# Optimization experiments

Measured on AMD Instinct MI355X. Metric: run time of the kernel, lower is better.

The kernel has to match this reference:

```python
import jax, jax.numpy as jnp
import numpy as np

EPS = 1e-7


def ciou_pairwise(b1, b2):
    # b1: (N,1,4), b2: (1,N,4) in xyxy; returns (N,N) CIoU
    b1x1, b1y1, b1x2, b1y2 = b1[..., 0], b1[..., 1], b1[..., 2], b1[..., 3]
    b2x1, b2y1, b2x2, b2y2 = b2[..., 0], b2[..., 1], b2[..., 2], b2[..., 3]

    # intersection
    iw = jnp.clip(jnp.minimum(b1x2, b2x2) - jnp.maximum(b1x1, b2x1), 0.0)
    ih = jnp.clip(jnp.minimum(b1y2, b2y2) - jnp.maximum(b1y1, b2y1), 0.0)
    inter = iw * ih

    w1, h1 = b1x2 - b1x1, b1y2 - b1y1
    w2, h2 = b2x2 - b2x1, b2y2 - b2y1
    union = w1 * h1 + w2 * h2 - inter + EPS
    iou = inter / union

    # smallest enclosing box diagonal
    cw = jnp.maximum(b1x2, b2x2) - jnp.minimum(b1x1, b2x1)
    ch = jnp.maximum(b1y2, b2y2) - jnp.minimum(b1y1, b2y1)
    c2 = cw * cw + ch * ch + EPS

    # squared center distance
    rho2 = ((b2x1 + b2x2 - b1x1 - b1x2) ** 2 + (b2y1 + b2y2 - b1y1 - b1y2) ** 2) / 4.0

    # aspect-ratio consistency term
    v = (4.0 / (np.pi ** 2)) * (jnp.arctan(w2 / (h2 + EPS)) - jnp.arctan(w1 / (h1 + EPS))) ** 2
    alpha = jax.lax.stop_gradient(v / (v - iou + (1.0 + EPS)))
    return iou - (rho2 / c2 + v * alpha)


def setup_inputs() -> dict:
    key = jax.random.key(0)
    k1, k2, k3 = jax.random.split(key, 3)
    N = 4096
    conf = jax.random.uniform(k1, (N, 1), dtype=jnp.float32)           # confidence in [0,1)
    xy1 = jax.random.uniform(k2, (N, 2), dtype=jnp.float32) * 600.0    # top-left corner
    wh = jax.random.uniform(k3, (N, 2), dtype=jnp.float32) * 100.0 + 1.0  # width/height >= 1
    x = jnp.concatenate([conf, xy1, xy1 + wh], axis=1)                 # (N, 5): conf, x1, y1, x2, y2
    gamma = jnp.zeros((1,), dtype=jnp.float32)
    return {"x": x, "gamma": gamma}


def reference(x, gamma):
    boxes = x[:, 1:]
    conf = x[:, 0]
    iou = ciou_pairwise(boxes[:, None, :], boxes[None, :, :])          # (N, N)
    conf_matrix = conf[:, None] * conf[None, :]                        # (N, N) outer product
    attention = jax.nn.softmax(iou * conf_matrix, axis=-1)             # (N, N)
    x_prime = x * gamma + attention @ x                                # (N, 5)
    return jax.nn.sigmoid(x_prime)
```

## Files before the change

kernel.cpp:

```cpp
#include <hip/hip_runtime.h>
#include <math.h>

#define N 4096
#define FEPS 1e-7f
#define HEPS 5e-8f
#define BLK 256
#define JT 64
#define CH 64
#define NPAIR (CH / 2)
#define KATAN 0.6366197723675814f
#define SQL2E 1.2011224087864498f

typedef float v2f __attribute__((ext_vector_type(2)));


__device__ __forceinline__ v2f min2(v2f a, v2f b) {
    v2f r; r.x = fminf(a.x, b.x); r.y = fminf(a.y, b.y); return r;
}
__device__ __forceinline__ v2f max2(v2f a, v2f b) {
    v2f r; r.x = fmaxf(a.x, b.x); r.y = fmaxf(a.y, b.y); return r;
}
__device__ __forceinline__ v2f rcp2(v2f a) {
    v2f r; r.x = __builtin_amdgcn_rcpf(a.x); r.y = __builtin_amdgcn_rcpf(a.y); return r;
}
__device__ __forceinline__ v2f exp22(v2f a) {
    v2f r; r.x = __builtin_amdgcn_exp2f(a.x); r.y = __builtin_amdgcn_exp2f(a.y); return r;
}

__global__ __launch_bounds__(BLK) void ciou_attn_kernel(
        const float* __restrict__ x,
        float* __restrict__ part) {
    __shared__ float jrec[NPAIR * 24];
    const int tid = threadIdx.x;
    const int gb = blockIdx.x / JT;
    const int jt = blockIdx.x % JT;
    const int i = gb * BLK + tid;

    if (tid < CH) {
        int j = jt * CH + tid;
        float cf = x[j * 5 + 0], jx1 = x[j * 5 + 1], jy1 = x[j * 5 + 2];
        float jx2 = x[j * 5 + 3], jy2 = x[j * 5 + 4];
        float w = jx2 - jx1, h = jy2 - jy1;
        float* dp = &jrec[(tid >> 1) * 24 + (tid & 1)];
        dp[0]  = jx1;               dp[2]  = jy1;
        dp[4]  = jx2;               dp[6]  = jy2;
        dp[8]  = (jx1 + jx2) * 0.5f; dp[10] = (jy1 + jy2) * 0.5f;
        dp[12] = w;                 dp[14] = h;
        dp[16] = fmaf(w, h, HEPS);
        dp[18] = KATAN * atanf(w / (h + FEPS));
        dp[20] = cf * SQL2E;        dp[22] = cf;
    }

    const float rx1 = x[i * 5 + 1], ry1 = x[i * 5 + 2];
    const float rx2 = x[i * 5 + 3], ry2 = x[i * 5 + 4];
    const float rw = rx2 - rx1, rh = ry2 - ry1;
    const float rhx = (rx1 + rx2) * 0.5f, rhy = (ry1 + ry2) * 0.5f;
    const float rareps = fmaf(rw, rh, HEPS);
    const float rat = KATAN * atanf(rw / (rh + FEPS));
    const float rcf2 = x[i * 5 + 0] * SQL2E;

    __syncthreads();

    v2f sum = 0.f, a0 = 0.f, a1 = 0.f, a2 = 0.f, a3 = 0.f, a4 = 0.f;
    const float ONEP = 1.f + FEPS;

#pragma unroll 4
    for (int p = 0; p < NPAIR; p++) {
        const float* f = &jrec[p * 24];
        const v2f X1 = *(const v2f*)(f + 0),  Y1 = *(const v2f*)(f + 2);
        const v2f X2 = *(const v2f*)(f + 4),  Y2 = *(const v2f*)(f + 6);
        const v2f HX = *(const v2f*)(f + 8),  HY = *(const v2f*)(f + 10);
        const v2f W  = *(const v2f*)(f + 12), H  = *(const v2f*)(f + 14);
        const v2f AR = *(const v2f*)(f + 16), AT = *(const v2f*)(f + 18);
        const v2f CF2 = *(const v2f*)(f + 20), CF = *(const v2f*)(f + 22);

        v2f iwr = min2(rx2, X2) - max2(rx1, X1);
        v2f ihr = min2(ry2, Y2) - max2(ry1, Y1);
        v2f inter = max2(iwr, 0.f) * max2(ihr, 0.f);
        v2f uni = (rareps + AR) - inter;
        v2f cw = (rw + W) - iwr;
        v2f chh = (rh + H) - ihr;
        v2f c2 = cw * cw + chh * chh + FEPS;
        v2f dx = HX - rhx;
        v2f dy = HY - rhy;
        v2f rho2 = dx * dx + dy * dy;
        v2f da = AT - rat;
        v2f v = da * da;
        v2f P = (v + ONEP) * uni - inter;
        P = max2(P, 1e-12f);
        v2f rr = rcp2(uni * c2 * P);
        v2f t1 = inter * c2 - rho2 * uni;
        v2f vu = v * uni;
        v2f num = t1 * P - (vu * vu) * c2;
        v2f e = exp22((num * rr) * (rcf2 * CF2));
        sum += e;
        a0 += e * CF;
        a1 += e * X1;
        a2 += e * Y1;
        a3 += e * X2;
        a4 += e * Y2;
    }

    float* p = part + (size_t)jt * 6 * N;
    p[0 * N + i] = sum.x + sum.y;
    p[1 * N + i] = a0.x + a0.y;
    p[2 * N + i] = a1.x + a1.y;
    p[3 * N + i] = a2.x + a2.y;
    p[4 * N + i] = a3.x + a3.y;
    p[5 * N + i] = a4.x + a4.y;
}

__global__ void epilogue_kernel(const float* __restrict__ x,
                                const float* __restrict__ gamma,
                                const float* __restrict__ part,
                                float* __restrict__ out) {
    int idx = blockIdx.x * blockDim.x + threadIdx.x;
    if (idx >= N * 5) return;
    int c = idx / N, i = idx - c * N;
    float se = 0.f, a = 0.f;
#pragma unroll 8
    for (int jt = 0; jt < JT; jt++) {
        const float* p = part + (size_t)jt * 6 * N;
        se += p[0 * N + i];
        a  += p[(1 + c) * N + i];
    }
    float xp = x[i * 5 + c] * gamma[0] + a / se;
    out[i * 5 + c] = 1.f / (1.f + expf(-xp));
}

extern "C" void kernel_launch(void* const* d_in, const int* in_sizes, int n_in,
                              void* d_out, int out_size, void* d_ws, size_t ws_size,
                              hipStream_t stream) {
    const float* x = (const float*)d_in[0];
    const float* gamma = (const float*)d_in[1];
    float* out = (float*)d_out;
    float* part = (float*)d_ws;

    ciou_attn_kernel<<<(N / BLK) * JT, BLK, 0, stream>>>(x, part);
    epilogue_kernel<<<(N * 5 + 255) / 256, 256, 0, stream>>>(x, gamma, part, out);
}
```

Measured before the change: 81.27 us.

## Shrink shared j-record and split epilogue reduction across four waves

The per-j shared-memory record is reduced from 12 to 6 pairs. Width, height, centre and area are now recomputed in the inner loop from the corner coordinates, and the raw confidence is recovered by rescaling the pre-scaled one after the loop. This trades a few extra ALU ops per pair for fewer LDS reads. The epilogue now splits the 64 partial tiles across four waves per output group and combines them with a shared-memory reduction, which adds parallelism and memory-level concurrency to the partial sums.

Measured after the change: 77.47 us (median of 2 runs). 4.7% less time.

```diff
diff --git a/kernel.cpp b/kernel.cpp
--- a/kernel.cpp
+++ b/kernel.cpp
@@ -10,6 +10,7 @@
 #define NPAIR (CH / 2)
 #define KATAN 0.6366197723675814f
 #define SQL2E 1.2011224087864498f
+#define ISQL2E 0.8325546111576977f
 
 typedef float v2f __attribute__((ext_vector_type(2)));
 
@@ -30,7 +31,7 @@
 __global__ __launch_bounds__(BLK) void ciou_attn_kernel(
         const float* __restrict__ x,
         float* __restrict__ part) {
-    __shared__ float jrec[NPAIR * 24];
+    __shared__ float jrec[NPAIR * 12];
     const int tid = threadIdx.x;
     const int gb = blockIdx.x / JT;
     const int jt = blockIdx.x % JT;
@@ -40,15 +41,10 @@
         int j = jt * CH + tid;
         float cf = x[j * 5 + 0], jx1 = x[j * 5 + 1], jy1 = x[j * 5 + 2];
         float jx2 = x[j * 5 + 3], jy2 = x[j * 5 + 4];
-        float w = jx2 - jx1, h = jy2 - jy1;
-        float* dp = &jrec[(tid >> 1) * 24 + (tid & 1)];
-        dp[0]  = jx1;               dp[2]  = jy1;
-        dp[4]  = jx2;               dp[6]  = jy2;
-        dp[8]  = (jx1 + jx2) * 0.5f; dp[10] = (jy1 + jy2) * 0.5f;
-        dp[12] = w;                 dp[14] = h;
-        dp[16] = fmaf(w, h, HEPS);
-        dp[18] = KATAN * atanf(w / (h + FEPS));
-        dp[20] = cf * SQL2E;        dp[22] = cf;
+        float* dp = &jrec[(tid >> 1) * 12 + (tid & 1)];
+        dp[0]  = jx1;  dp[2] = jy1;  dp[4] = jx2;  dp[6] = jy2;
+        dp[8]  = KATAN * atanf((jx2 - jx1) / ((jy2 - jy1) + FEPS));
+        dp[10] = cf * SQL2E;
     }
 
     const float rx1 = x[i * 5 + 1], ry1 = x[i * 5 + 2];
@@ -66,13 +62,13 @@
 
 #pragma unroll 4
     for (int p = 0; p < NPAIR; p++) {
-        const float* f = &jrec[p * 24];
+        const float* f = &jrec[p * 12];
         const v2f X1 = *(const v2f*)(f + 0),  Y1 = *(const v2f*)(f + 2);
         const v2f X2 = *(const v2f*)(f + 4),  Y2 = *(const v2f*)(f + 6);
-        const v2f HX = *(const v2f*)(f + 8),  HY = *(const v2f*)(f + 10);
-        const v2f W  = *(const v2f*)(f + 12), H  = *(const v2f*)(f + 14);
-        const v2f AR = *(const v2f*)(f + 16), AT = *(const v2f*)(f + 18);
-        const v2f CF2 = *(const v2f*)(f + 20), CF = *(const v2f*)(f + 22);
+        const v2f AT = *(const v2f*)(f + 8),  CF2 = *(const v2f*)(f + 10);
+        const v2f W = X2 - X1, H = Y2 - Y1;
+        const v2f HX = (X1 + X2) * 0.5f, HY = (Y1 + Y2) * 0.5f;
+        const v2f AR = W * H + HEPS;
 
         v2f iwr = min2(rx2, X2) - max2(rx1, X1);
         v2f ihr = min2(ry2, Y2) - max2(ry1, Y1);
@@ -94,7 +90,7 @@
         v2f num = t1 * P - (vu * vu) * c2;
         v2f e = exp22((num * rr) * (rcf2 * CF2));
         sum += e;
-        a0 += e * CF;
+        a0 += e * CF2;
         a1 += e * X1;
         a2 += e * Y1;
         a3 += e * X2;
@@ -103,7 +99,7 @@
 
     float* p = part + (size_t)jt * 6 * N;
     p[0 * N + i] = sum.x + sum.y;
-    p[1 * N + i] = a0.x + a0.y;
+    p[1 * N + i] = (a0.x + a0.y) * ISQL2E;
     p[2 * N + i] = a1.x + a1.y;
     p[3 * N + i] = a2.x + a2.y;
     p[4 * N + i] = a3.x + a3.y;
@@ -114,18 +110,27 @@
                                 const float* __restrict__ gamma,
                                 const float* __restrict__ part,
                                 float* __restrict__ out) {
-    int idx = blockIdx.x * blockDim.x + threadIdx.x;
-    if (idx >= N * 5) return;
-    int c = idx / N, i = idx - c * N;
+    __shared__ float red[2][BLK];
+    const int t = threadIdx.x;
+    const int o = t & 63, q = t >> 6;
+    const int idx = blockIdx.x * 64 + o;
+    const int c = idx / N, i = idx - c * N;
     float se = 0.f, a = 0.f;
-#pragma unroll 8
-    for (int jt = 0; jt < JT; jt++) {
-        const float* p = part + (size_t)jt * 6 * N;
+    const float* ps = part + (size_t)(q * 16) * 6 * N;
+#pragma unroll
+    for (int k = 0; k < 16; k++) {
+        const float* p = ps + (size_t)k * 6 * N;
         se += p[0 * N + i];
         a  += p[(1 + c) * N + i];
     }
-    float xp = x[i * 5 + c] * gamma[0] + a / se;
-    out[i * 5 + c] = 1.f / (1.f + expf(-xp));
+    red[0][t] = se; red[1][t] = a;
+    __syncthreads();
+    if (t < 64) {
+        float se4 = (red[0][t] + red[0][t + 64]) + (red[0][t + 128] + red[0][t + 192]);
+        float a4  = (red[1][t] + red[1][t + 64]) + (red[1][t + 128] + red[1][t + 192]);
+        float xp = x[i * 5 + c] * gamma[0] + a4 / se4;
+        out[i * 5 + c] = 1.f / (1.f + expf(-xp));
+    }
 }
 
 extern "C" void kernel_launch(void* const* d_in, const int* in_sizes, int n_in,
@@ -137,5 +142,5 @@
     float* part = (float*)d_ws;
 
     ciou_attn_kernel<<<(N / BLK) * JT, BLK, 0, stream>>>(x, part);
-    epilogue_kernel<<<(N * 5 + 255) / 256, 256, 0, stream>>>(x, gamma, part, out);
+    epilogue_kernel<<<(N * 5) / 64, BLK, 0, stream>>>(x, gamma, part, out);
 }
```
